# Performance work log

Measured on AMD Instinct MI355X. Metric: run time of the kernel, lower is better.

Reference implementation:

```python
import jax, jax.numpy as jnp
import numpy as np

HEAD_NUM = 16

def setup_inputs() -> dict:
    key = jax.random.key(0)
    kq, kk, kv = jax.random.split(key, 3)
    shape = (4, 2048, 1024)  # [B, N, C]
    return {
        "query_layer": jax.random.normal(kq, shape, dtype=jnp.float32),
        "key_layer": jax.random.normal(kk, shape, dtype=jnp.float32),
        "value_layer": jax.random.normal(kv, shape, dtype=jnp.float32),
    }

def _split_heads(x, h):
    B, N, C = x.shape
    return x.reshape(B, N, h, C // h).transpose(0, 2, 1, 3)  # [B,H,N,d]

def reference(query_layer, key_layer, value_layer):
    B, N, C = query_layer.shape
    h = HEAD_NUM
    d = C // h
    q = _split_heads(query_layer, h)
    k = _split_heads(key_layer, h)
    v = _split_heads(value_layer, h)
    scores = jnp.einsum('bhnd,bhmd->bhnm', q, k) / jnp.sqrt(jnp.asarray(d, q.dtype))
    probs = jax.nn.softmax(scores, axis=-1)
    ctx = jnp.einsum('bhnm,bhmd->bhnd', probs, v)
    return ctx.transpose(0, 2, 1, 3).reshape(B, N, C)
```

## Files before the change

### kernel.cpp

```cpp
#include <hip/hip_runtime.h>
#include <hip/hip_bf16.h>

#define B_   4
#define N_   2048
#define C_   1024
#define NT   32
#define QSCALE 0.18033688011112042f

typedef __attribute__((ext_vector_type(8)))  short short8;
typedef __attribute__((ext_vector_type(4)))  float f32x4;
typedef __attribute__((ext_vector_type(16))) float f32x16;
typedef __attribute__((ext_vector_type(2)))  int   int2v;

__device__ __forceinline__ unsigned short f2bf(float x) {
    union { __hip_bfloat16 h; unsigned short u; } c;
    c.h = __float2bfloat16(x);
    return c.u;
}
__device__ __forceinline__ float fast_exp2(float x) {
    float r; asm("v_exp_f32 %0, %1" : "=v"(r) : "v"(x)); return r;
}
__device__ __forceinline__ int cvtpk(float a, float b) {
    int r; asm("v_cvt_pk_bf16_f32 %0, %1, %2" : "=v"(r) : "v"(a), "v"(b)); return r;
}

__global__ __launch_bounds__(256) void prepack(
    const float* __restrict__ K, const float* __restrict__ V,
    unsigned short* __restrict__ Kt, unsigned short* __restrict__ Vt)
{
    __shared__ __align__(16) unsigned short kl[4096];
    __shared__ __align__(16) unsigned short vl[4096];
    const int L = blockIdx.x;
    const int xcd = L & 7;
    const int j = L >> 3;
    const int head = xcd + 8 * (j >> 5);
    const int t = j & 31;
    const int b = head >> 4, h = head & 15;
    const int tid = threadIdx.x;
    const int r = tid >> 2, cb = tid & 3;
    const size_t head_off = (size_t)b * N_ * C_ + (size_t)h * 64;
    const int kv0 = t * 64;
    const int blk_out = head * NT + t;

    {
        const float* src = K + head_off + (size_t)(kv0 + r) * C_ + cb * 16;
        f32x4 x0 = *(const f32x4*)(src);
        f32x4 x1 = *(const f32x4*)(src + 4);
        f32x4 x2 = *(const f32x4*)(src + 8);
        f32x4 x3 = *(const f32x4*)(src + 12);
        short8 p0, p1;
        #pragma unroll
        for (int i = 0; i < 4; ++i) {
            p0[i] = (short)f2bf(x0[i]); p0[i + 4] = (short)f2bf(x1[i]);
            p1[i] = (short)f2bf(x2[i]); p1[i + 4] = (short)f2bf(x3[i]);
        }
        const int swz = (r & 7) << 3;
        *(short8*)&kl[r * 64 + ((cb * 16) ^ swz)]     = p0;
        *(short8*)&kl[r * 64 + ((cb * 16 + 8) ^ swz)] = p1;
    }
    {
        const float* src = V + head_off + (size_t)(kv0 + r) * C_ + cb * 16;
        f32x4 y0 = *(const f32x4*)(src);
        f32x4 y1 = *(const f32x4*)(src + 4);
        f32x4 y2 = *(const f32x4*)(src + 8);
        f32x4 y3 = *(const f32x4*)(src + 12);
        #pragma unroll
        for (int i = 0; i < 4; ++i) {
            int d0 = cb * 16 + i;
            vl[d0 * 64 + (r ^ ((d0 & 7) << 3))] = f2bf(y0[i]);
            int d1 = cb * 16 + 4 + i;
            vl[d1 * 64 + (r ^ ((d1 & 7) << 3))] = f2bf(y1[i]);
            int d2 = cb * 16 + 8 + i;
            vl[d2 * 64 + (r ^ ((d2 & 7) << 3))] = f2bf(y2[i]);
            int d3 = cb * 16 + 12 + i;
            vl[d3 * 64 + (r ^ ((d3 & 7) << 3))] = f2bf(y3[i]);
        }
    }
    __syncthreads();
    #pragma unroll
    for (int cc = 0; cc < 2; ++cc) {
        const int c  = tid + cc * 256;
        const int f  = c >> 6;
        const int ln = c & 63;
        const int row = (f & 1) * 32 + (ln & 31);
        const int col = (f >> 1) * 16 + (ln >> 5) * 8;
        const int sw  = (row & 7) << 3;
        short8 kk = *(const short8*)&kl[row * 64 + (col ^ sw)];
        short8 vv = *(const short8*)&vl[row * 64 + (col ^ sw)];
        *(short8*)&Kt[(size_t)blk_out * 4096 + c * 8] = kk;
        *(short8*)&Vt[(size_t)blk_out * 4096 + c * 8] = vv;
    }
}

__global__ __launch_bounds__(256, 4) void attn_fwd(
    const float* __restrict__ Q, const unsigned short* __restrict__ Kt,
    const unsigned short* __restrict__ Vt, float* __restrict__ O)
{
    __shared__ __align__(16) unsigned short klds[2][4096];
    __shared__ __align__(16) unsigned short vlds[2][4096];

    const int L = blockIdx.x;
    const int xcd = L & 7;
    const int j = L >> 3;
    const int head = xcd + 8 * (j >> 4);
    const int qt = j & 15;
    const int b = head >> 4, h = head & 15;

    const int tid  = threadIdx.x;
    const int wave = tid >> 6;
    const int lane = tid & 63;
    const int l31  = lane & 31;
    const int hi   = lane >> 5;

    const unsigned short* kbase = Kt + (size_t)head * (NT * 4096);
    const unsigned short* vbase = Vt + (size_t)head * (NT * 4096);
    const float* qp = Q + (size_t)b * N_ * C_ + (size_t)h * 64;
    float*       op = O + (size_t)b * N_ * C_ + (size_t)h * 64;

    const int qrow = qt * 128 + wave * 32 + l31;
    short8 qfrag[4];
    {
        const float* qr = qp + (size_t)qrow * C_ + hi * 8;
        #pragma unroll
        for (int ks = 0; ks < 4; ++ks) {
            f32x4 x0 = *(const f32x4*)(qr + ks * 16);
            f32x4 x1 = *(const f32x4*)(qr + ks * 16 + 4);
            short8 a;
            #pragma unroll
            for (int i = 0; i < 4; ++i) {
                a[i]     = (short)f2bf(x0[i] * QSCALE);
                a[i + 4] = (short)f2bf(x1[i] * QSCALE);
            }
            qfrag[ks] = a;
        }
    }

    f32x16 o0 = {}, o1 = {};
    float m_r = -3.0e38f, l_r = 0.0f;

    const int lofs = lane * 8;

    auto stage = [&](int t, int buf) {
        const unsigned short* kg = kbase + (size_t)t * 4096 + wave * 1024 + lofs;
        const unsigned short* vg = vbase + (size_t)t * 4096 + wave * 1024 + lofs;
        __builtin_amdgcn_global_load_lds((const __attribute__((address_space(1))) void*)kg,
            (__attribute__((address_space(3))) void*)&klds[buf][wave * 1024], 16, 0, 0);
        __builtin_amdgcn_global_load_lds((const __attribute__((address_space(1))) void*)(kg + 512),
            (__attribute__((address_space(3))) void*)&klds[buf][wave * 1024 + 512], 16, 0, 0);
        __builtin_amdgcn_global_load_lds((const __attribute__((address_space(1))) void*)vg,
            (__attribute__((address_space(3))) void*)&vlds[buf][wave * 1024], 16, 0, 0);
        __builtin_amdgcn_global_load_lds((const __attribute__((address_space(1))) void*)(vg + 512),
            (__attribute__((address_space(3))) void*)&vlds[buf][wave * 1024 + 512], 16, 0, 0);
    };

    stage(0, 0);
    int cur = 0;

    for (int t = 0; t < NT; ++t) {
        asm volatile("s_waitcnt vmcnt(0)" ::: "memory");
        __syncthreads();
        if (t + 1 < NT) stage(t + 1, cur ^ 1);

        const unsigned short* kl = klds[cur];
        const unsigned short* vl = vlds[cur];

        f32x16 s0 = {}, s1 = {};
        __builtin_amdgcn_s_setprio(1);
        #pragma unroll
        for (int ks = 0; ks < 4; ++ks) {
            short8 kf0 = *(const short8*)&kl[ks * 1024 + lofs];
            short8 kf1 = *(const short8*)&kl[ks * 1024 + 512 + lofs];
            s0 = __builtin_amdgcn_mfma_f32_32x32x16_bf16(kf0, qfrag[ks], s0, 0, 0, 0);
            s1 = __builtin_amdgcn_mfma_f32_32x32x16_bf16(kf1, qfrag[ks], s1, 0, 0, 0);
        }
        __builtin_amdgcn_s_setprio(0);

        float mx[8];
        #pragma unroll
        for (int r = 0; r < 8; ++r) mx[r] = fmaxf(fmaxf(s0[r], s0[r + 8]), fmaxf(s1[r], s1[r + 8]));
        #pragma unroll
        for (int st = 4; st; st >>= 1) {
            #pragma unroll
            for (int r = 0; r < st; ++r) mx[r] = fmaxf(mx[r], mx[r + st]);
        }
        int2v msw = __builtin_amdgcn_permlane32_swap(__float_as_int(mx[0]), __float_as_int(mx[0]), false, false);
        const float rm = fmaxf(__int_as_float(msw[0]), __int_as_float(msw[1]));

        if (!__all(rm - m_r <= 8.0f)) {
            const float mnew = fmaxf(m_r, rm);
            const float corr = fast_exp2(m_r - mnew);
            m_r = mnew;
            l_r *= corr;
            #pragma unroll
            for (int r = 0; r < 16; ++r) { o0[r] *= corr; o1[r] *= corr; }
        }

        #pragma unroll
        for (int r = 0; r < 16; ++r) {
            s0[r] = fast_exp2(s0[r] - m_r);
            s1[r] = fast_exp2(s1[r] - m_r);
        }
        float aa[8];
        #pragma unroll
        for (int r = 0; r < 8; ++r) aa[r] = (s0[r] + s0[r + 8]) + (s1[r] + s1[r + 8]);
        #pragma unroll
        for (int st = 4; st; st >>= 1) {
            #pragma unroll
            for (int r = 0; r < st; ++r) aa[r] += aa[r + st];
        }
        int2v ssw = __builtin_amdgcn_permlane32_swap(__float_as_int(aa[0]), __float_as_int(aa[0]), false, false);
        l_r += __int_as_float(ssw[0]) + __int_as_float(ssw[1]);

        short8 pf[4];
        #pragma unroll
        for (int ct = 0; ct < 2; ++ct) {
            #pragma unroll
            for (int kss = 0; kss < 2; ++kss) {
                float e0, e1, e2, e3, e4, e5, e6, e7;
                if (ct == 0) {
                    e0 = s0[8*kss+0]; e1 = s0[8*kss+1]; e2 = s0[8*kss+2]; e3 = s0[8*kss+3];
                    e4 = s0[8*kss+4]; e5 = s0[8*kss+5]; e6 = s0[8*kss+6]; e7 = s0[8*kss+7];
                } else {
                    e0 = s1[8*kss+0]; e1 = s1[8*kss+1]; e2 = s1[8*kss+2]; e3 = s1[8*kss+3];
                    e4 = s1[8*kss+4]; e5 = s1[8*kss+5]; e6 = s1[8*kss+6]; e7 = s1[8*kss+7];
                }
                int w0 = cvtpk(e0, e1);
                int w1 = cvtpk(e2, e3);
                int w2 = cvtpk(e4, e5);
                int w3 = cvtpk(e6, e7);
                int2v sA = __builtin_amdgcn_permlane32_swap(w0, w2, false, false);
                int2v sB = __builtin_amdgcn_permlane32_swap(w1, w3, false, false);
                union { int i[4]; short8 v; } u;
                u.i[0] = sA[0]; u.i[1] = sB[0]; u.i[2] = sA[1]; u.i[3] = sB[1];
                pf[ct * 2 + kss] = u.v;
            }
        }

        __builtin_amdgcn_s_setprio(1);
        #pragma unroll
        for (int ks = 0; ks < 4; ++ks) {
            short8 vf0 = *(const short8*)&vl[ks * 1024 + lofs];
            short8 vf1 = *(const short8*)&vl[ks * 1024 + 512 + lofs];
            o0 = __builtin_amdgcn_mfma_f32_32x32x16_bf16(vf0, pf[ks], o0, 0, 0, 0);
            o1 = __builtin_amdgcn_mfma_f32_32x32x16_bf16(vf1, pf[ks], o1, 0, 0, 0);
        }
        __builtin_amdgcn_s_setprio(0);

        cur ^= 1;
    }

    const float inv = 1.0f / l_r;
    float* orow = op + (size_t)qrow * C_;
    #pragma unroll
    for (int bb = 0; bb < 4; ++bb) {
        f32x4 w0, w1;
        #pragma unroll
        for (int i = 0; i < 4; ++i) {
            w0[i] = o0[4 * bb + i] * inv;
            w1[i] = o1[4 * bb + i] * inv;
        }
        *(f32x4*)(orow + 8 * bb + 4 * hi)      = w0;
        *(f32x4*)(orow + 32 + 8 * bb + 4 * hi) = w1;
    }
}

extern "C" void kernel_launch(void* const* d_in, const int* in_sizes, int n_in,
                              void* d_out, int out_size, void* d_ws, size_t ws_size,
                              hipStream_t stream) {
    const float* q = (const float*)d_in[0];
    const float* k = (const float*)d_in[1];
    const float* v = (const float*)d_in[2];
    float* o = (float*)d_out;
    unsigned short* Kt = (unsigned short*)d_ws;
    unsigned short* Vt = Kt + (size_t)64 * NT * 4096;
    prepack<<<dim3(64 * NT), dim3(256), 0, stream>>>(k, v, Kt, Vt);
    attn_fwd<<<dim3(1024), dim3(256), 0, stream>>>(q, Kt, Vt, o);
}
```

Measured before the change: 111.5 us.

## Load V fragments directly from global into registers instead of LDS

V tiles are no longer staged through double-buffered LDS. Each wave now reads its V MFMA operands straight from global memory into registers, with half issued before the QK^T MFMAs and half before the PV MFMAs. This halves LDS usage and removes the V LDS writes and reads, and the top-of-loop waitcnt/barrier is replaced by one barrier at the end of the iteration. In exchange, every wave fetches the full V tile, quadrupling V cache traffic, and register pressure rises. Because memory counters are in-order, waiting on the V loads also waits on the K prefetch issued before them.

```diff
diff --git a/kernel.cpp b/kernel.cpp
--- a/kernel.cpp
+++ b/kernel.cpp
@@ -97,7 +97,6 @@
     const unsigned short* __restrict__ Vt, float* __restrict__ O)
 {
     __shared__ __align__(16) unsigned short klds[2][4096];
-    __shared__ __align__(16) unsigned short vlds[2][4096];
 
     const int L = blockIdx.x;
     const int xcd = L & 7;
@@ -140,29 +139,28 @@
 
     const int lofs = lane * 8;
 
-    auto stage = [&](int t, int buf) {
+    auto stageK = [&](int t, int buf) {
         const unsigned short* kg = kbase + (size_t)t * 4096 + wave * 1024 + lofs;
-        const unsigned short* vg = vbase + (size_t)t * 4096 + wave * 1024 + lofs;
         __builtin_amdgcn_global_load_lds((const __attribute__((address_space(1))) void*)kg,
             (__attribute__((address_space(3))) void*)&klds[buf][wave * 1024], 16, 0, 0);
         __builtin_amdgcn_global_load_lds((const __attribute__((address_space(1))) void*)(kg + 512),
             (__attribute__((address_space(3))) void*)&klds[buf][wave * 1024 + 512], 16, 0, 0);
-        __builtin_amdgcn_global_load_lds((const __attribute__((address_space(1))) void*)vg,
-            (__attribute__((address_space(3))) void*)&vlds[buf][wave * 1024], 16, 0, 0);
-        __builtin_amdgcn_global_load_lds((const __attribute__((address_space(1))) void*)(vg + 512),
-            (__attribute__((address_space(3))) void*)&vlds[buf][wave * 1024 + 512], 16, 0, 0);
     };
 
-    stage(0, 0);
+    stageK(0, 0);
+    __syncthreads();
     int cur = 0;
 
     for (int t = 0; t < NT; ++t) {
-        asm volatile("s_waitcnt vmcnt(0)" ::: "memory");
-        __syncthreads();
-        if (t + 1 < NT) stage(t + 1, cur ^ 1);
+        if (t + 1 < NT) stageK(t + 1, cur ^ 1);
+
+        const unsigned short* vtp = vbase + (size_t)t * 4096 + lofs;
+        short8 vA0 = *(const short8*)(vtp);
+        short8 vA1 = *(const short8*)(vtp + 512);
+        short8 vA2 = *(const short8*)(vtp + 1024);
+        short8 vA3 = *(const short8*)(vtp + 1536);
 
         const unsigned short* kl = klds[cur];
-        const unsigned short* vl = vlds[cur];
 
         f32x16 s0 = {}, s1 = {};
         __builtin_amdgcn_s_setprio(1);
@@ -236,16 +234,23 @@
             }
         }
 
+        short8 vB0 = *(const short8*)(vtp + 2048);
+        short8 vB1 = *(const short8*)(vtp + 2560);
+        short8 vB2 = *(const short8*)(vtp + 3072);
+        short8 vB3 = *(const short8*)(vtp + 3584);
+
         __builtin_amdgcn_s_setprio(1);
-        #pragma unroll
-        for (int ks = 0; ks < 4; ++ks) {
-            short8 vf0 = *(const short8*)&vl[ks * 1024 + lofs];
-            short8 vf1 = *(const short8*)&vl[ks * 1024 + 512 + lofs];
-            o0 = __builtin_amdgcn_mfma_f32_32x32x16_bf16(vf0, pf[ks], o0, 0, 0, 0);
-            o1 = __builtin_amdgcn_mfma_f32_32x32x16_bf16(vf1, pf[ks], o1, 0, 0, 0);
-        }
+        o0 = __builtin_amdgcn_mfma_f32_32x32x16_bf16(vA0, pf[0], o0, 0, 0, 0);
+        o1 = __builtin_amdgcn_mfma_f32_32x32x16_bf16(vA1, pf[0], o1, 0, 0, 0);
+        o0 = __builtin_amdgcn_mfma_f32_32x32x16_bf16(vA2, pf[1], o0, 0, 0, 0);
+        o1 = __builtin_amdgcn_mfma_f32_32x32x16_bf16(vA3, pf[1], o1, 0, 0, 0);
+        o0 = __builtin_amdgcn_mfma_f32_32x32x16_bf16(vB0, pf[2], o0, 0, 0, 0);
+        o1 = __builtin_amdgcn_mfma_f32_32x32x16_bf16(vB1, pf[2], o1, 0, 0, 0);
+        o0 = __builtin_amdgcn_mfma_f32_32x32x16_bf16(vB2, pf[3], o0, 0, 0, 0);
+        o1 = __builtin_amdgcn_mfma_f32_32x32x16_bf16(vB3, pf[3], o1, 0, 0, 0);
         __builtin_amdgcn_s_setprio(0);
 
+        __syncthreads();
         cur ^= 1;
     }
 
```

Result: slower. 113.7 us (+2.0%).
